# Kernel optimization log

Measured on AMD Instinct MI355X. Metric: run time of the kernel, lower is better.

## Reference

```python
import jax, jax.numpy as jnp
import numpy as np

N_NODES = 100000
N_EDGES = 1000000
IN_CH = 312
HID = 256
OUT = 256


def _sage_conv(x, src, dst, W_l, b_l, W_r, num_nodes):
    # PyG SAGEConv (mean aggr): out = mean_{j in N(i)} x_j @ W_l + b_l + x_i @ W_r
    msg = x[src]                                             # [E, C] gather
    agg = jax.ops.segment_sum(msg, dst, num_segments=num_nodes)  # [N, C]
    deg = jax.ops.segment_sum(jnp.ones((src.shape[0],), dtype=x.dtype), dst,
                              num_segments=num_nodes)        # [N]
    mean = agg / jnp.maximum(deg, 1.0)[:, None]
    return mean @ W_l + b_l + x @ W_r


def setup_inputs() -> dict:
    key = jax.random.key(0)
    ks = jax.random.split(key, 8)
    x = jax.random.normal(ks[0], (N_NODES, IN_CH), dtype=jnp.float32)
    edge_index = jax.random.randint(ks[1], (2, N_EDGES), 0, N_NODES, dtype=jnp.int64)
    s1 = 1.0 / np.sqrt(IN_CH)
    s2 = 1.0 / np.sqrt(HID)
    W1_l = jax.random.normal(ks[2], (IN_CH, HID), dtype=jnp.float32) * s1
    b1 = jnp.zeros((HID,), dtype=jnp.float32)
    W1_r = jax.random.normal(ks[3], (IN_CH, HID), dtype=jnp.float32) * s1
    W2_l = jax.random.normal(ks[4], (HID, OUT), dtype=jnp.float32) * s2
    b2 = jnp.zeros((OUT,), dtype=jnp.float32)
    W2_r = jax.random.normal(ks[5], (HID, OUT), dtype=jnp.float32) * s2
    return {"x": x, "edge_index": edge_index, "W1_l": W1_l, "b1": b1,
            "W1_r": W1_r, "W2_l": W2_l, "b2": b2, "W2_r": W2_r}


def reference(x, edge_index, W1_l, b1, W1_r, W2_l, b2, W2_r):
    src, dst = edge_index[0], edge_index[1]
    n = x.shape[0]
    h = _sage_conv(x, src, dst, W1_l, b1, W1_r, n)
    h = jax.nn.relu(h)
    out = _sage_conv(h, src, dst, W2_l, b2, W2_r, n)
    return out
```

## Files before the change

### kernel.cpp

```cpp
#include <hip/hip_runtime.h>
#include <hip/hip_bf16.h>
#include <cstdint>
#include <cstddef>

#define IN_CH 312
#define HID 256

typedef __attribute__((ext_vector_type(8))) short bf16x8;
typedef __attribute__((ext_vector_type(4))) float f32x4;
typedef __attribute__((ext_vector_type(8))) unsigned short ushort8;

__device__ __forceinline__ unsigned short f2bf(float f) {
    union { float f; unsigned u; } v; v.f = f;
    const unsigned r = v.u + 0x7FFFu + ((v.u >> 16) & 1u);
    return (unsigned short)(r >> 16);
}
__device__ __forceinline__ float bf2f(unsigned short s) {
    union { unsigned u; float f; } v; v.u = (unsigned)s << 16;
    return v.f;
}
__device__ __forceinline__ void gload_lds16(const void* g, void* l) {
    __builtin_amdgcn_global_load_lds(
        (const __attribute__((address_space(1))) void*)g,
        (__attribute__((address_space(3))) void*)l, 16, 0, 0);
}

__global__ void detect_idx_kernel(const void* __restrict__ ei, int* __restrict__ flag) {
    if (blockIdx.x == 0 && threadIdx.x == 0) {
        const int* p = (const int*)ei;
        int ok = 1;
        for (int i = 0; i < 64; ++i) ok &= (p[2 * i + 1] == 0);
        *flag = ok;
    }
}
__device__ __forceinline__ long long load_idx(const void* ei, long long i, bool is64) {
    return is64 ? ((const long long*)ei)[i] : (long long)((const int*)ei)[i];
}

__global__ void hist_kernel(const void* __restrict__ ei, const int* __restrict__ flag,
                            int* __restrict__ cnt, int E) {
    const int i = blockIdx.x * blockDim.x + threadIdx.x;
    if (i >= E) return;
    const bool is64 = (*flag != 0);
    atomicAdd(&cnt[load_idx(ei, (long long)E + i, is64)], 1);
}

__global__ void offsets_kernel(const int* __restrict__ cnt, int* __restrict__ counter,
                               int* __restrict__ beg, int* __restrict__ cur, int n) {
    const int i = blockIdx.x * blockDim.x + threadIdx.x;
    if (i >= n) return;
    const int b = atomicAdd(counter, cnt[i]);
    beg[i] = b;
    cur[i] = b;
}

__global__ void fill_kernel(const void* __restrict__ ei, const int* __restrict__ flag,
                            int* __restrict__ cur, int* __restrict__ col, int E) {
    const int i = blockIdx.x * blockDim.x + threadIdx.x;
    if (i >= E) return;
    const bool is64 = (*flag != 0);
    const long long s = load_idx(ei, i, is64);
    const long long d = load_idx(ei, (long long)E + i, is64);
    col[atomicAdd(&cur[d], 1)] = (int)s;
}

__global__ void convert_x_kernel(const float* __restrict__ x, unsigned short* __restrict__ xb,
                                 int N) {
    const int tid = blockIdx.x * blockDim.x + threadIdx.x;
    if (tid >= N * 40) return;
    const int row = tid / 40;
    const int c8 = (tid % 40) * 8;
    ushort8 o;
    if (c8 < IN_CH) {
        const float4 v0 = *(const float4*)(x + (size_t)row * IN_CH + c8);
        const float4 v1 = *(const float4*)(x + (size_t)row * IN_CH + c8 + 4);
        o[0] = f2bf(v0.x); o[1] = f2bf(v0.y); o[2] = f2bf(v0.z); o[3] = f2bf(v0.w);
        o[4] = f2bf(v1.x); o[5] = f2bf(v1.y); o[6] = f2bf(v1.z); o[7] = f2bf(v1.w);
    } else {
        o = (ushort8)0;
    }
    *(ushort8*)(xb + (size_t)row * 320 + c8) = o;
}

__global__ void convert_w_kernel(const float* __restrict__ Wl, const float* __restrict__ Wr,
                                 unsigned short* __restrict__ wt, int K, int Kpad) {
    const int tid = blockIdx.x * blockDim.x + threadIdx.x;
    if (tid >= 512 * Kpad) return;
    const int c = tid / Kpad;
    const int k = tid % Kpad;
    float v = 0.f;
    if (k < K) v = (c < 256) ? Wl[(size_t)k * 256 + c] : Wr[(size_t)k * 256 + (c - 256)];
    wt[(size_t)c * Kpad + k] = f2bf(v);
}

template <int KPAD, int ZSTR>
__global__ __launch_bounds__(512) void mfma_gemm_kernel(
    const unsigned short* __restrict__ A,
    const unsigned short* __restrict__ WT,
    const float* __restrict__ bias,
    unsigned short* __restrict__ Y,
    unsigned short* __restrict__ Z,
    int M)
{
    constexpr int NS = KPAD / 32;
    __shared__ __align__(16) char smem[49152];

    const int tid  = (int)threadIdx.x;
    const int lane = tid & 63;
    const int wid  = tid >> 6;
    const int wr = wid >> 1, wc = wid & 1;
    const int r0 = blockIdx.x * 128;
    const int c0 = blockIdx.y * 256;

    const int lrow = lane & 15;
    const int kgrp = lane >> 4;

    f32x4 acc[2][8];
    #pragma unroll
    for (int i = 0; i < 2; ++i)
        #pragma unroll
        for (int j = 0; j < 8; ++j) acc[i][j] = (f32x4)0.f;

    const int glrow = lane >> 2;
    const int glc   = (lane & 3) ^ ((glrow >> 1) & 3);

    auto stage = [&](int t, int b) {
        char* ab = smem + b * 8192;
        char* bb = smem + 16384 + b * 16384;
        const int kb = t * 32;
        #pragma unroll
        for (int j = 0; j < 2; ++j) {
            const int ld = wid * 2 + j;
            const int row = ld * 16 + glrow;
            gload_lds16(WT + (size_t)(c0 + row) * KPAD + kb + glc * 8,
                        bb + ld * 1024);
        }
        const int arow = wid * 16 + glrow;
        const int gr = min(r0 + arow, M - 1);
        gload_lds16(A + (size_t)gr * KPAD + kb + glc * 8, ab + wid * 1024);
    };
    auto compute = [&](int b) {
        const char* ab = smem + b * 8192;
        const char* bb = smem + 16384 + b * 16384;
        bf16x8 af[2], bg[8];
        #pragma unroll
        for (int f = 0; f < 2; ++f) {
            const int arow = wr * 32 + f * 16 + lrow;
            const int p = kgrp ^ ((arow >> 1) & 3);
            af[f] = *(const bf16x8*)(ab + arow * 64 + p * 16);
        }
        #pragma unroll
        for (int fn = 0; fn < 8; ++fn) {
            const int brow = wc * 128 + fn * 16 + lrow;
            const int p = kgrp ^ ((brow >> 1) & 3);
            bg[fn] = *(const bf16x8*)(bb + brow * 64 + p * 16);
        }
        #pragma unroll
        for (int fn = 0; fn < 8; ++fn) {
            acc[0][fn] = __builtin_amdgcn_mfma_f32_16x16x32_bf16(af[0], bg[fn], acc[0][fn], 0, 0, 0);
            acc[1][fn] = __builtin_amdgcn_mfma_f32_16x16x32_bf16(af[1], bg[fn], acc[1][fn], 0, 0, 0);
        }
    };

    stage(0, 0);
    __builtin_amdgcn_sched_barrier(0);
    asm volatile("" ::: "memory");
    stage(1, 1);
    __builtin_amdgcn_sched_barrier(0);
    asm volatile("" ::: "memory");

    #pragma unroll
    for (int t = 0; t < NS; ++t) {
        const int b = t & 1;
        if (t + 1 < NS) {
            asm volatile("s_waitcnt vmcnt(3)" ::: "memory");
        } else {
            asm volatile("s_waitcnt vmcnt(0)" ::: "memory");
        }
        asm volatile("s_barrier" ::: "memory");
        __builtin_amdgcn_sched_barrier(0);
        compute(b);
        if (t + 2 < NS) {
            asm volatile("s_waitcnt lgkmcnt(0)\n\ts_barrier" ::: "memory");
            stage(t + 2, b);
        }
    }

    const bool isY = (c0 == 0);
    const int cloc = wc * 128 + (lane & 15);

    constexpr int CST = 264;
    short* c_lds = (short*)smem;
    float bv4[8];
    #pragma unroll
    for (int fn = 0; fn < 8; ++fn)
        bv4[fn] = isY ? 0.f : bias[cloc + fn * 16];
    #pragma unroll
    for (int h = 0; h < 2; ++h) {
        __syncthreads();
        if ((wr >> 1) == h) {
            const int lr0 = (wr & 1) * 32 + (lane >> 4) * 4;
            #pragma unroll
            for (int fm = 0; fm < 2; ++fm)
                #pragma unroll
                for (int fn = 0; fn < 8; ++fn)
                    #pragma unroll
                    for (int r = 0; r < 4; ++r)
                        c_lds[(lr0 + fm * 16 + r) * CST + cloc + fn * 16] =
                            (short)f2bf(acc[fm][fn][r] + bv4[fn]);
        }
        __syncthreads();
        const int row = tid >> 3;
        const int cb  = (tid & 7) * 32;
        const int gr  = r0 + h * 64 + row;
        if (gr < M) {
            unsigned short* dst = isY
                ? (Y + (size_t)gr * 256 + cb)
                : (Z + (size_t)gr * ZSTR + cb);
            #pragma unroll
            for (int j = 0; j < 4; ++j)
                *(ushort8*)(dst + j * 8) =
                    *(const ushort8*)&c_lds[row * CST + cb + j * 8];
        }
    }
}

template <bool LAYER1>
__global__ void gather_agg_kernel(const unsigned short* __restrict__ Y,
                                  const int* __restrict__ beg_arr,
                                  const int* __restrict__ cnt,
                                  const int* __restrict__ col,
                                  const unsigned short* Z,
                                  void* OUT, int N)
{
    const long long gw = ((long long)blockIdx.x * blockDim.x + threadIdx.x) >> 6;
    if (gw >= N) return;
    const int w = (int)gw;
    const int lane = threadIdx.x & 63;
    const int c4 = lane * 4;
    const int beg = beg_arr[w];
    const int deg = cnt[w];
    const int end = beg + deg;

    const size_t zstr = LAYER1 ? 256 : 512;
    const ushort4 zb = *(const ushort4*)(Z + (size_t)w * zstr + c4);
    const float4 z = make_float4(bf2f(zb.x), bf2f(zb.y), bf2f(zb.z), bf2f(zb.w));

    float4 a0 = make_float4(0.f, 0.f, 0.f, 0.f);
    float4 a1 = make_float4(0.f, 0.f, 0.f, 0.f);
    int e = beg;
    for (; e + 3 < end; e += 4) {
        const int s0 = col[e], s1 = col[e + 1], s2 = col[e + 2], s3 = col[e + 3];
        const ushort4 v0 = *(const ushort4*)(Y + (size_t)s0 * 256 + c4);
        const ushort4 v1 = *(const ushort4*)(Y + (size_t)s1 * 256 + c4);
        const ushort4 v2 = *(const ushort4*)(Y + (size_t)s2 * 256 + c4);
        const ushort4 v3 = *(const ushort4*)(Y + (size_t)s3 * 256 + c4);
        a0.x += bf2f(v0.x) + bf2f(v1.x);  a1.x += bf2f(v2.x) + bf2f(v3.x);
        a0.y += bf2f(v0.y) + bf2f(v1.y);  a1.y += bf2f(v2.y) + bf2f(v3.y);
        a0.z += bf2f(v0.z) + bf2f(v1.z);  a1.z += bf2f(v2.z) + bf2f(v3.z);
        a0.w += bf2f(v0.w) + bf2f(v1.w);  a1.w += bf2f(v2.w) + bf2f(v3.w);
    }
    if (e + 1 < end) {
        const int s0 = col[e], s1 = col[e + 1];
        const ushort4 v0 = *(const ushort4*)(Y + (size_t)s0 * 256 + c4);
        const ushort4 v1 = *(const ushort4*)(Y + (size_t)s1 * 256 + c4);
        a0.x += bf2f(v0.x) + bf2f(v1.x);
        a0.y += bf2f(v0.y) + bf2f(v1.y);
        a0.z += bf2f(v0.z) + bf2f(v1.z);
        a0.w += bf2f(v0.w) + bf2f(v1.w);
        e += 2;
    }
    if (e < end) {
        const ushort4 v0 = *(const ushort4*)(Y + (size_t)col[e] * 256 + c4);
        a0.x += bf2f(v0.x); a0.y += bf2f(v0.y);
        a0.z += bf2f(v0.z); a0.w += bf2f(v0.w);
    }
    float4 acc;
    acc.x = a0.x + a1.x; acc.y = a0.y + a1.y;
    acc.z = a0.z + a1.z; acc.w = a0.w + a1.w;

    const float inv = 1.0f / fmaxf((float)deg, 1.0f);
    float4 o;
    o.x = acc.x * inv + z.x;
    o.y = acc.y * inv + z.y;
    o.z = acc.z * inv + z.z;
    o.w = acc.w * inv + z.w;
    if (LAYER1) {
        o.x = fmaxf(o.x, 0.f); o.y = fmaxf(o.y, 0.f);
        o.z = fmaxf(o.z, 0.f); o.w = fmaxf(o.w, 0.f);
        ushort4 ob;
        ob.x = f2bf(o.x); ob.y = f2bf(o.y); ob.z = f2bf(o.z); ob.w = f2bf(o.w);
        *(ushort4*)((unsigned short*)OUT + (size_t)w * 256 + c4) = ob;
    } else {
        *(float4*)((float*)OUT + (size_t)w * 256 + c4) = o;
    }
}

extern "C" void kernel_launch(void* const* d_in, const int* in_sizes, int n_in,
                              void* d_out, int out_size, void* d_ws, size_t ws_size,
                              hipStream_t stream) {
    const float* x   = (const float*)d_in[0];
    const void*  ei  = d_in[1];
    const float* W1l = (const float*)d_in[2];
    const float* b1  = (const float*)d_in[3];
    const float* W1r = (const float*)d_in[4];
    const float* W2l = (const float*)d_in[5];
    const float* b2  = (const float*)d_in[6];
    const float* W2r = (const float*)d_in[7];

    const int N = in_sizes[0] / IN_CH;
    const int E = in_sizes[1] / 2;

    char* ws = (char*)d_ws;
    size_t off = 0;
    auto alloc = [&](size_t bytes) {
        void* p = ws + off;
        off = (off + bytes + 255) & ~(size_t)255;
        return p;
    };
    int* flag    = (int*)alloc(4);
    int* cnt     = (int*)alloc((size_t)(N + 1) * 4);
    int* counter = cnt + N;
    int* beg     = (int*)alloc((size_t)N * 4);
    int* cur     = (int*)alloc((size_t)N * 4);
    int* col     = (int*)alloc((size_t)E * 4);
    unsigned short* wt1 = (unsigned short*)alloc((size_t)512 * 320 * 2);
    unsigned short* wt2 = (unsigned short*)alloc((size_t)512 * 256 * 2);
    unsigned short* xb  = (unsigned short*)alloc((size_t)N * 320 * 2);
    unsigned short* y   = (unsigned short*)alloc((size_t)N * 256 * 2);

    unsigned short* hb = xb;

    float* out = (float*)d_out;
    unsigned short* z1 = (unsigned short*)d_out;
    unsigned short* z2 = (unsigned short*)d_out;

    hipMemsetAsync(cnt, 0, (size_t)(N + 1) * 4, stream);
    detect_idx_kernel<<<1, 64, 0, stream>>>(ei, flag);
    hist_kernel<<<(E + 255) / 256, 256, 0, stream>>>(ei, flag, cnt, E);
    offsets_kernel<<<(N + 255) / 256, 256, 0, stream>>>(cnt, counter, beg, cur, N);
    fill_kernel<<<(E + 255) / 256, 256, 0, stream>>>(ei, flag, cur, col, E);

    convert_x_kernel<<<(N * 40 + 255) / 256, 256, 0, stream>>>(x, xb, N);
    convert_w_kernel<<<(512 * 320 + 255) / 256, 256, 0, stream>>>(W1l, W1r, wt1, IN_CH, 320);
    convert_w_kernel<<<(512 * 256 + 255) / 256, 256, 0, stream>>>(W2l, W2r, wt2, HID, 256);

    const dim3 ggrid((N + 127) / 128, 2);

    mfma_gemm_kernel<320, 256><<<ggrid, 512, 0, stream>>>(xb, wt1, b1, y, z1, N);
    gather_agg_kernel<true><<<(N + 3) / 4, 256, 0, stream>>>(y, beg, cnt, col, z1, hb, N);

    mfma_gemm_kernel<256, 512><<<ggrid, 512, 0, stream>>>(hb, wt2, b2, y, z2, N);
    gather_agg_kernel<false><<<(N + 3) / 4, 256, 0, stream>>>(y, beg, cnt, col, z2, out, N);
}
```

Baseline: 460.6 us.

## Split gather features into two column-half planes and aggregate each half separately

New measurement: 495.3 us. +7.5%, slower.

```diff
diff --git a/kernel.cpp b/kernel.cpp
--- a/kernel.cpp
+++ b/kernel.cpp
@@ -215,7 +215,7 @@
         const int gr  = r0 + h * 64 + row;
         if (gr < M) {
             unsigned short* dst = isY
-                ? (Y + (size_t)gr * 256 + cb)
+                ? (Y + (size_t)(cb >> 7) * ((size_t)M * 128) + (size_t)gr * 128 + (cb & 127))
                 : (Z + (size_t)gr * ZSTR + cb);
             #pragma unroll
             for (int j = 0; j < 4; ++j)
@@ -231,68 +231,57 @@
                                   const int* __restrict__ cnt,
                                   const int* __restrict__ col,
                                   const unsigned short* Z,
-                                  void* OUT, int N)
+                                  void* OUT, int N, int half)
 {
     const long long gw = ((long long)blockIdx.x * blockDim.x + threadIdx.x) >> 6;
     if (gw >= N) return;
     const int w = (int)gw;
     const int lane = threadIdx.x & 63;
-    const int c4 = lane * 4;
+    const int c2 = lane * 2;
     const int beg = beg_arr[w];
     const int deg = cnt[w];
     const int end = beg + deg;
 
+    const unsigned short* yh = Y + (size_t)half * ((size_t)N * 128);
+
     const size_t zstr = LAYER1 ? 256 : 512;
-    const ushort4 zb = *(const ushort4*)(Z + (size_t)w * zstr + c4);
-    const float4 z = make_float4(bf2f(zb.x), bf2f(zb.y), bf2f(zb.z), bf2f(zb.w));
-
-    float4 a0 = make_float4(0.f, 0.f, 0.f, 0.f);
-    float4 a1 = make_float4(0.f, 0.f, 0.f, 0.f);
+    const ushort2 zb = *(const ushort2*)(Z + (size_t)w * zstr + half * 128 + c2);
+    const float zx = bf2f(zb.x), zy = bf2f(zb.y);
+
+    float a0x = 0.f, a0y = 0.f, a1x = 0.f, a1y = 0.f;
     int e = beg;
     for (; e + 3 < end; e += 4) {
         const int s0 = col[e], s1 = col[e + 1], s2 = col[e + 2], s3 = col[e + 3];
-        const ushort4 v0 = *(const ushort4*)(Y + (size_t)s0 * 256 + c4);
-        const ushort4 v1 = *(const ushort4*)(Y + (size_t)s1 * 256 + c4);
-        const ushort4 v2 = *(const ushort4*)(Y + (size_t)s2 * 256 + c4);
-        const ushort4 v3 = *(const ushort4*)(Y + (size_t)s3 * 256 + c4);
-        a0.x += bf2f(v0.x) + bf2f(v1.x);  a1.x += bf2f(v2.x) + bf2f(v3.x);
-        a0.y += bf2f(v0.y) + bf2f(v1.y);  a1.y += bf2f(v2.y) + bf2f(v3.y);
-        a0.z += bf2f(v0.z) + bf2f(v1.z);  a1.z += bf2f(v2.z) + bf2f(v3.z);
-        a0.w += bf2f(v0.w) + bf2f(v1.w);  a1.w += bf2f(v2.w) + bf2f(v3.w);
+        const ushort2 v0 = *(const ushort2*)(yh + (size_t)s0 * 128 + c2);
+        const ushort2 v1 = *(const ushort2*)(yh + (size_t)s1 * 128 + c2);
+        const ushort2 v2 = *(const ushort2*)(yh + (size_t)s2 * 128 + c2);
+        const ushort2 v3 = *(const ushort2*)(yh + (size_t)s3 * 128 + c2);
+        a0x += bf2f(v0.x) + bf2f(v1.x);  a1x += bf2f(v2.x) + bf2f(v3.x);
+        a0y += bf2f(v0.y) + bf2f(v1.y);  a1y += bf2f(v2.y) + bf2f(v3.y);
     }
     if (e + 1 < end) {
         const int s0 = col[e], s1 = col[e + 1];
-        const ushort4 v0 = *(const ushort4*)(Y + (size_t)s0 * 256 + c4);
-        const ushort4 v1 = *(const ushort4*)(Y + (size_t)s1 * 256 + c4);
-        a0.x += bf2f(v0.x) + bf2f(v1.x);
-        a0.y += bf2f(v0.y) + bf2f(v1.y);
-        a0.z += bf2f(v0.z) + bf2f(v1.z);
-        a0.w += bf2f(v0.w) + bf2f(v1.w);
+        const ushort2 v0 = *(const ushort2*)(yh + (size_t)s0 * 128 + c2);
+        const ushort2 v1 = *(const ushort2*)(yh + (size_t)s1 * 128 + c2);
+        a0x += bf2f(v0.x) + bf2f(v1.x);
+        a0y += bf2f(v0.y) + bf2f(v1.y);
         e += 2;
     }
     if (e < end) {
-        const ushort4 v0 = *(const ushort4*)(Y + (size_t)col[e] * 256 + c4);
-        a0.x += bf2f(v0.x); a0.y += bf2f(v0.y);
-        a0.z += bf2f(v0.z); a0.w += bf2f(v0.w);
-    }
-    float4 acc;
-    acc.x = a0.x + a1.x; acc.y = a0.y + a1.y;
-    acc.z = a0.z + a1.z; acc.w = a0.w + a1.w;
+        const ushort2 v0 = *(const ushort2*)(yh + (size_t)col[e] * 128 + c2);
+        a0x += bf2f(v0.x); a0y += bf2f(v0.y);
+    }
 
     const float inv = 1.0f / fmaxf((float)deg, 1.0f);
-    float4 o;
-    o.x = acc.x * inv + z.x;
-    o.y = acc.y * inv + z.y;
-    o.z = acc.z * inv + z.z;
-    o.w = acc.w * inv + z.w;
+    float ox = (a0x + a1x) * inv + zx;
+    float oy = (a0y + a1y) * inv + zy;
     if (LAYER1) {
-        o.x = fmaxf(o.x, 0.f); o.y = fmaxf(o.y, 0.f);
-        o.z = fmaxf(o.z, 0.f); o.w = fmaxf(o.w, 0.f);
-        ushort4 ob;
-        ob.x = f2bf(o.x); ob.y = f2bf(o.y); ob.z = f2bf(o.z); ob.w = f2bf(o.w);
-        *(ushort4*)((unsigned short*)OUT + (size_t)w * 256 + c4) = ob;
+        ox = fmaxf(ox, 0.f); oy = fmaxf(oy, 0.f);
+        ushort2 ob; ob.x = f2bf(ox); ob.y = f2bf(oy);
+        *(ushort2*)((unsigned short*)OUT + (size_t)w * 256 + half * 128 + c2) = ob;
     } else {
-        *(float4*)((float*)OUT + (size_t)w * 256 + c4) = o;
+        float2 of; of.x = ox; of.y = oy;
+        *(float2*)((float*)OUT + (size_t)w * 256 + half * 128 + c2) = of;
     }
 }
 
@@ -333,7 +322,7 @@
 
     float* out = (float*)d_out;
     unsigned short* z1 = (unsigned short*)d_out;
-    unsigned short* z2 = (unsigned short*)d_out;
+    unsigned short* z2 = (unsigned short*)d_out + 256;
 
     hipMemsetAsync(cnt, 0, (size_t)(N + 1) * 4, stream);
     detect_idx_kernel<<<1, 64, 0, stream>>>(ei, flag);
@@ -346,10 +335,13 @@
     convert_w_kernel<<<(512 * 256 + 255) / 256, 256, 0, stream>>>(W2l, W2r, wt2, HID, 256);
 
     const dim3 ggrid((N + 127) / 128, 2);
+    const int gblocks = (N + 3) / 4;
 
     mfma_gemm_kernel<320, 256><<<ggrid, 512, 0, stream>>>(xb, wt1, b1, y, z1, N);
-    gather_agg_kernel<true><<<(N + 3) / 4, 256, 0, stream>>>(y, beg, cnt, col, z1, hb, N);
+    gather_agg_kernel<true><<<gblocks, 256, 0, stream>>>(y, beg, cnt, col, z1, hb, N, 0);
+    gather_agg_kernel<true><<<gblocks, 256, 0, stream>>>(y, beg, cnt, col, z1, hb, N, 1);
 
     mfma_gemm_kernel<256, 512><<<ggrid, 512, 0, stream>>>(hb, wt2, b2, y, z2, N);
-    gather_agg_kernel<false><<<(N + 3) / 4, 256, 0, stream>>>(y, beg, cnt, col, z2, out, N);
-}
+    gather_agg_kernel<false><<<gblocks, 256, 0, stream>>>(y, beg, cnt, col, z2, out, N, 0);
+    gather_agg_kernel<false><<<gblocks, 256, 0, stream>>>(y, beg, cnt, col, z2, out, N, 1);
+}
```
